# Kernel tuning notes

Hardware: AMD Instinct MI355X
Metric: run time of the kernel (lower is better)

## Reference

```python
import jax, jax.numpy as jnp
import numpy as np

DIM = 512
NUM_HEADS = 8
HEAD_DIM = DIM // NUM_HEADS
EPS = 1e-05
BETA_INIT, TEMP_INIT, SHARP_INIT = 1.0, 0.5, 4.0


def setup_inputs() -> dict:
    key = jax.random.key(0)
    ks = jax.random.split(key, 9)
    b, t = 2, 1024
    s = 1.0 / np.sqrt(DIM)
    inp = {
        "x": jax.random.normal(ks[0], (b, t, DIM), dtype=jnp.float32),
        "wq_k": jax.random.normal(ks[1], (DIM, DIM), dtype=jnp.float32) * s,
        "wq_b": jnp.zeros((DIM,), dtype=jnp.float32),
        "wk_k": jax.random.normal(ks[2], (DIM, DIM), dtype=jnp.float32) * s,
        "wk_b": jnp.zeros((DIM,), dtype=jnp.float32),
        "wv_k": jax.random.normal(ks[3], (DIM, DIM), dtype=jnp.float32) * s,
        "wv_b": jnp.zeros((DIM,), dtype=jnp.float32),
        "wo_k": jax.random.normal(ks[4], (DIM, DIM), dtype=jnp.float32) * s,
        "wo_b": jnp.zeros((DIM,), dtype=jnp.float32),
        "log_beta": jnp.full((NUM_HEADS,), np.log(BETA_INIT), dtype=jnp.float32),
        "log_temp": jnp.full((NUM_HEADS,), np.log(TEMP_INIT), dtype=jnp.float32),
        "log_sharp": jnp.full((NUM_HEADS,), np.log(SHARP_INIT), dtype=jnp.float32),
    }
    return inp


def _softplus(x, beta):
    return (1.0 / beta) * jnp.log(1.0 + jnp.exp(beta * x))


def _combine(a, b):
    # log-domain combine: elements m (b,h,t,n), log_N (b,h,t,p,n), log_D (b,h,t,n)
    m_x, ln_x, ld_x = a
    m_y, ln_y, ld_y = b
    m_new = jnp.maximum(m_x, m_y)
    dx = m_x - m_new
    dy = m_y - m_new
    # note: (..., None) broadcast onto (b,h,t,p,n) works because p == n == HEAD_DIM
    ln_new = jnp.logaddexp(ln_x + dx[..., None], ln_y + dy[..., None])
    ld_new = jnp.logaddexp(ld_x + dx, ld_y + dy)
    return (m_new, ln_new, ld_new)


def reference(x, wq_k, wq_b, wk_k, wk_b, wv_k, wv_b, wo_k, wo_b,
              log_beta, log_temp, log_sharp):
    b, t, _ = x.shape
    q = (x @ wq_k + wq_b).reshape(b, t, NUM_HEADS, HEAD_DIM).transpose(0, 2, 1, 3)
    k = (x @ wk_k + wk_b).reshape(b, t, NUM_HEADS, HEAD_DIM).transpose(0, 2, 1, 3)
    v = (x @ wv_k + wv_b).reshape(b, t, NUM_HEADS, HEAD_DIM).transpose(0, 2, 1, 3)

    beta = jnp.exp(log_beta)[:, None, None]   # (h,1,1)
    temp = jnp.exp(log_temp)[:, None, None]
    sharp = jnp.exp(log_sharp)[:, None, None]

    q = q / temp
    k = k / temp
    Qf = _softplus(q, beta)  # (b,h,t,n)
    Kf = _softplus(k, beta)

    m0 = jnp.log(Kf + EPS)                         # (b,h,t,n)
    N0 = jnp.einsum('bhtp,bhtn->bhtpn', v, Kf)     # (b,h,t,p,n)
    D0 = Kf                                        # (b,h,t,n)

    m_c, N_c, D_c = jax.lax.associative_scan(_combine, (m0, N0, D0), axis=2)

    Y_num = jnp.einsum('bhtp,bhtpq->bhtq', Qf, N_c)
    Y_den = jnp.einsum('bhtp,bhtp->bht', Qf, D_c)
    Y = Y_num / (Y_den[..., None] + EPS)           # (b,h,t,n)
    Y = jnp.sign(Y) * jnp.abs(Y) ** sharp

    pos = (jnp.arange(1, t + 1, dtype=Y.dtype) / t).reshape(1, 1, t, 1)
    Y = Y * pos

    Y = Y.transpose(0, 2, 1, 3).reshape(b, t, DIM)
    return Y @ wo_k + wo_b
```

## Files before the change

### kernel.cpp

```cpp
#include <hip/hip_runtime.h>
#include <hip/hip_bf16.h>
#include <math.h>

#define DIM 512
#define NH 8
#define HD 64
#define TT 1024
#define CH 64
#define CL 16
#define EPSF 1e-5f
#define LN2F 0.69314718056f
#define LOG2EF 1.44269504089f

typedef unsigned short ushort_t;
typedef __attribute__((ext_vector_type(8))) short bf16x8;
typedef __attribute__((ext_vector_type(4))) float f32x4;

__device__ __forceinline__ float fexp2(float x) { return __builtin_amdgcn_exp2f(x); }
__device__ __forceinline__ float flog2(float x) { return __builtin_amdgcn_logf(x); }

__device__ __forceinline__ ushort_t f2bf(float f) {
    union { float f; unsigned u; } v; v.f = f;
    unsigned r = v.u + 0x7FFFu + ((v.u >> 16) & 1u);
    return (ushort_t)(r >> 16);
}
__device__ __forceinline__ float bf2f(ushort_t h) {
    union { unsigned u; float f; } v; v.u = ((unsigned)h) << 16;
    return v.f;
}

__launch_bounds__(256)
__global__ void k_cvt_x(const float* __restrict__ x, ushort_t* __restrict__ xh,
                        ushort_t* __restrict__ xl)
{
    int i = (blockIdx.x * 256 + threadIdx.x) * 4;
    float4 v = *(const float4*)&x[i];
    ushort4 h, l;
    h.x = f2bf(v.x); l.x = f2bf(v.x - bf2f(h.x));
    h.y = f2bf(v.y); l.y = f2bf(v.y - bf2f(h.y));
    h.z = f2bf(v.z); l.z = f2bf(v.z - bf2f(h.z));
    h.w = f2bf(v.w); l.w = f2bf(v.w - bf2f(h.w));
    *(ushort4*)&xh[i] = h;
    *(ushort4*)&xl[i] = l;
}

__launch_bounds__(256)
__global__ void k_cvt_w(const float* __restrict__ wq, const float* __restrict__ wk,
                        const float* __restrict__ wv, const float* __restrict__ wo,
                        ushort_t* __restrict__ wTh, ushort_t* __restrict__ wTl,
                        ushort_t* __restrict__ wTo)
{
    const int mat = blockIdx.z;
    const float* w = (mat == 0) ? wq : (mat == 1) ? wk : (mat == 2) ? wv : wo;
    const int n  = blockIdx.x * 64 + (threadIdx.x & 63);
    const int k0 = blockIdx.y * 128 + (threadIdx.x >> 6) * 32;

    ushort_t hb[32], lb[32];
#pragma unroll
    for (int j = 0; j < 32; j++) {
        float v = w[(size_t)(k0 + j) * DIM + n];
        hb[j] = f2bf(v);
        lb[j] = f2bf(v - bf2f(hb[j]));
    }
    if (mat < 3) {
        ushort_t* dh = wTh + (size_t)mat * DIM * DIM + (size_t)n * DIM + k0;
        ushort_t* dl = wTl + (size_t)mat * DIM * DIM + (size_t)n * DIM + k0;
#pragma unroll
        for (int j = 0; j < 8; j++) {
            ushort4 th = { hb[4*j], hb[4*j+1], hb[4*j+2], hb[4*j+3] };
            ushort4 tl = { lb[4*j], lb[4*j+1], lb[4*j+2], lb[4*j+3] };
            *(ushort4*)&dh[4*j] = th;
            *(ushort4*)&dl[4*j] = tl;
        }
    } else {
        ushort_t* dh = wTo + (size_t)n * DIM + k0;
#pragma unroll
        for (int j = 0; j < 8; j++) {
            ushort4 th = { hb[4*j], hb[4*j+1], hb[4*j+2], hb[4*j+3] };
            *(ushort4*)&dh[4*j] = th;
        }
    }
}

__launch_bounds__(256, 4)
__global__ void k_gemm_qkv(const ushort_t* __restrict__ xh, const ushort_t* __restrict__ xl,
                           const ushort_t* __restrict__ wTh, const ushort_t* __restrict__ wTl,
                           const float* __restrict__ bq, const float* __restrict__ bk,
                           const float* __restrict__ bv,
                           const float* __restrict__ lbeta, const float* __restrict__ ltemp,
                           float* __restrict__ Qf2, float* __restrict__ Kf,
                           float* __restrict__ Vv2)
{
    const int z = blockIdx.z, h = blockIdx.x;
    const int rowBase = blockIdx.y * 64;
    const int colBase = h * 64;
    const float* bias = (z == 0) ? bq : (z == 1) ? bk : bv;

    __shared__ __align__(16) ushort_t lds[2][4][2048];

    const int tid = threadIdx.x;
    const int l = tid & 63, wv = tid >> 6;
    const int m = l & 15, g = l >> 4;

    const int rl = tid >> 2, cc = tid & 3;
    const int ci = ((rl >> 4) * 64 + cc * 16 + (rl & 15)) * 8;
    const ushort_t* gAh = xh + (size_t)(rowBase + rl) * DIM + cc * 8;
    const ushort_t* gAl = xl + (size_t)(rowBase + rl) * DIM + cc * 8;
    const ushort_t* gBh = wTh + (size_t)z * DIM * DIM + (size_t)(colBase + rl) * DIM + cc * 8;
    const ushort_t* gBl = wTl + (size_t)z * DIM * DIM + (size_t)(colBase + rl) * DIM + cc * 8;

    f32x4 acc[4] = { {0,0,0,0}, {0,0,0,0}, {0,0,0,0}, {0,0,0,0} };

    {
        bf16x8 a0 = *(const bf16x8*)gAh;
        bf16x8 a1 = *(const bf16x8*)gAl;
        bf16x8 b0 = *(const bf16x8*)gBh;
        bf16x8 b1 = *(const bf16x8*)gBl;
        *(bf16x8*)&lds[0][0][ci] = a0;
        *(bf16x8*)&lds[0][1][ci] = a1;
        *(bf16x8*)&lds[0][2][ci] = b0;
        *(bf16x8*)&lds[0][3][ci] = b1;
    }
    __syncthreads();

    for (int it = 0; it < 16; ++it) {
        const int cur = it & 1;
        bf16x8 nAh, nAl, nBh, nBl;
        if (it < 15) {
            const int K = (it + 1) * 32;
            nAh = *(const bf16x8*)(gAh + K);
            nAl = *(const bf16x8*)(gAl + K);
            nBh = *(const bf16x8*)(gBh + K);
            nBl = *(const bf16x8*)(gBl + K);
        }
        bf16x8 ah = *(const bf16x8*)&lds[cur][0][tid * 8];
        bf16x8 al = *(const bf16x8*)&lds[cur][1][tid * 8];
#pragma unroll
        for (int n = 0; n < 4; n++) {
            bf16x8 bh = *(const bf16x8*)&lds[cur][2][(n * 64 + l) * 8];
            bf16x8 bl = *(const bf16x8*)&lds[cur][3][(n * 64 + l) * 8];
            acc[n] = __builtin_amdgcn_mfma_f32_16x16x32_bf16(ah, bh, acc[n], 0, 0, 0);
            acc[n] = __builtin_amdgcn_mfma_f32_16x16x32_bf16(al, bh, acc[n], 0, 0, 0);
            acc[n] = __builtin_amdgcn_mfma_f32_16x16x32_bf16(ah, bl, acc[n], 0, 0, 0);
        }
        if (it < 15) {
            const int nxt = cur ^ 1;
            *(bf16x8*)&lds[nxt][0][ci] = nAh;
            *(bf16x8*)&lds[nxt][1][ci] = nAl;
            *(bf16x8*)&lds[nxt][2][ci] = nBh;
            *(bf16x8*)&lds[nxt][3][ci] = nBl;
            __syncthreads();
        }
    }

    if (z == 2) {
#pragma unroll
        for (int n = 0; n < 4; n++) {
            int c = n * 16 + m;
            float bval = bias[colBase + c];
#pragma unroll
            for (int r = 0; r < 4; r++) {
                int rr = rowBase + wv * 16 + g * 4 + r;
                int bb = rr >> 10, t = rr & (TT - 1);
                Vv2[(((size_t)(bb * NH + h)) * TT + t) * HD + c] = (acc[n][r] + bval) * LOG2EF;
            }
        }
    } else {
        float beta = expf(lbeta[h]);
        float itemp = 1.0f / expf(ltemp[h]);
        float oscale = (z == 0) ? (LN2F / beta) : (1.0f / beta);
        float* __restrict__ dst = (z == 0) ? Qf2 : Kf;
#pragma unroll
        for (int n = 0; n < 4; n++) {
            int c = n * 16 + m;
            float bval = bias[colBase + c];
#pragma unroll
            for (int r = 0; r < 4; r++) {
                int rr = rowBase + wv * 16 + g * 4 + r;
                int bb = rr >> 10, t = rr & (TT - 1);
                float val = (acc[n][r] + bval) * itemp;
                float zz = beta * val;
                float sp = (fmaxf(zz, 0.f) + log1pf(expf(-fabsf(zz)))) * oscale;
                dst[(((size_t)(bb * NH + h)) * TT + t) * HD + c] = sp;
            }
        }
    }
}

__launch_bounds__(256)
__global__ void k_chunk_reduce(const float* __restrict__ Kf, const float* __restrict__ Vv2,
                               float* __restrict__ aA, float* __restrict__ aD,
                               float* __restrict__ aCM)
{
    const int c = blockIdx.x >> 1, qh = blockIdx.x & 1;
    const int bh = blockIdx.z * NH + blockIdx.y;
    const int tid = threadIdx.x;

    __shared__ __align__(16) float sK[CL * HD];
    __shared__ __align__(16) float sV2[CL * HD];
    __shared__ __align__(16) float sM02[CL * HD];

    size_t base = ((size_t)bh * TT + (size_t)c * CL) * HD;
    const float4* K4 = (const float4*)(Kf + base);
    const float4* V4 = (const float4*)(Vv2 + base);
    {
        int f = tid;
        float4 kv = K4[f];
        ((float4*)sK)[f] = kv;
        float4 mm;
        mm.x = flog2(kv.x + EPSF); mm.y = flog2(kv.y + EPSF);
        mm.z = flog2(kv.z + EPSF); mm.w = flog2(kv.w + EPSF);
        ((float4*)sM02)[f] = mm;
        ((float4*)sV2)[f] = V4[f];
    }
    __syncthreads();

    const int p = tid & 63, qo = tid >> 6;
    const int q0 = qh * 32 + qo * 8;
    float A[8] = {};
    float AD = 0.f, cmx = 0.f;
    const bool doD = (qh == 0) && (tid < 64);

    for (int s = 0; s < CL; s++) {
        float vp = sV2[s * HD + p];
        float mp = sM02[s * HD + p];
        float4 ka = *(const float4*)&sK[s * HD + q0];
        float4 kb = *(const float4*)&sK[s * HD + q0 + 4];
        A[0] += fexp2(fmaf(vp, ka.x, mp));
        A[1] += fexp2(fmaf(vp, ka.y, mp));
        A[2] += fexp2(fmaf(vp, ka.z, mp));
        A[3] += fexp2(fmaf(vp, ka.w, mp));
        A[4] += fexp2(fmaf(vp, kb.x, mp));
        A[5] += fexp2(fmaf(vp, kb.y, mp));
        A[6] += fexp2(fmaf(vp, kb.z, mp));
        A[7] += fexp2(fmaf(vp, kb.w, mp));
        if (doD) {
            float kn = sK[s * HD + tid];
            float mn = sM02[s * HD + tid];
            AD += fexp2(fmaf(kn, LOG2EF, mn));
            cmx = fmaxf(cmx, kn + EPSF);
        }
    }

    size_t abase = ((size_t)bh * CH + c) * 4096 + (size_t)p * HD + q0;
    float4 o0 = { A[0], A[1], A[2], A[3] };
    float4 o1 = { A[4], A[5], A[6], A[7] };
    *(float4*)&aA[abase] = o0;
    *(float4*)&aA[abase + 4] = o1;
    if (doD) {
        size_t dbase = ((size_t)bh * CH + c) * HD + tid;
        aD[dbase] = AD; aCM[dbase] = cmx;
    }
}

__global__ void k_scan_agg(float* __restrict__ aA, float* __restrict__ aD,
                           float* __restrict__ aCM, int BH)
{
    int idx = blockIdx.x * 256 + threadIdx.x;
    int nA4 = BH * 1024;
    int nD4 = BH * 16;
    if (idx < nA4) {
        int bh = idx >> 10, pn4 = (idx & 1023) * 4;
        float4 Sr = {0.f, 0.f, 0.f, 0.f};
        for (int c = 0; c < CH; c++) {
            float* p = &aA[((size_t)bh * CH + c) * 4096 + pn4];
            float4 t = *(float4*)p;
            *(float4*)p = Sr;
            Sr.x += t.x; Sr.y += t.y; Sr.z += t.z; Sr.w += t.w;
        }
    } else if (idx < nA4 + nD4) {
        int i = idx - nA4; int bh = i >> 4, n4 = (i & 15) * 4;
        float4 Sr = {0.f, 0.f, 0.f, 0.f};
        for (int c = 0; c < CH; c++) {
            float* p = &aD[((size_t)bh * CH + c) * HD + n4];
            float4 t = *(float4*)p;
            *(float4*)p = Sr;
            Sr.x += t.x; Sr.y += t.y; Sr.z += t.z; Sr.w += t.w;
        }
    } else if (idx < nA4 + 2 * nD4) {
        int i = idx - nA4 - nD4; int bh = i >> 4, n4 = (i & 15) * 4;
        float4 r = {0.f, 0.f, 0.f, 0.f};
        for (int c = 0; c < CH; c++) {
            float* p = &aCM[((size_t)bh * CH + c) * HD + n4];
            float4 t = *(float4*)p;
            *(float4*)p = r;
            r.x = fmaxf(r.x, t.x); r.y = fmaxf(r.y, t.y);
            r.z = fmaxf(r.z, t.z); r.w = fmaxf(r.w, t.w);
        }
    }
}

__launch_bounds__(64)
__global__ void k_den(const float* __restrict__ Kf, const float* __restrict__ Qf2,
                      const float* __restrict__ aD, const float* __restrict__ aCM,
                      float* __restrict__ c1f, float* __restrict__ invd)
{
    const int c = blockIdx.x;
    const int bh = blockIdx.z * NH + blockIdx.y;
    const int n = threadIdx.x;
    size_t dbase = ((size_t)bh * CH + c) * HD + n;
    float AD = aD[dbase], cmx = aCM[dbase];
    size_t base = ((size_t)bh * TT + (size_t)c * CL) * HD + n;
    float* outc = c1f + (size_t)bh * TT + c * CL;
    float* outi = invd + (size_t)bh * TT + c * CL;

    for (int s = 0; s < CL; s++) {
        float kn = Kf[base + (size_t)s * HD];
        float qn = Qf2[base + (size_t)s * HD];
        float mn = flog2(kn + EPSF);
        AD += fexp2(fmaf(kn, LOG2EF, mn));
        cmx = fmaxf(cmx, kn + EPSF);
        float t1 = qn * flog2(cmx);
        float t2 = qn * flog2(AD);
#pragma unroll
        for (int off = 1; off <= 32; off <<= 1) {
            t1 += __shfl_xor(t1, off);
            t2 += __shfl_xor(t2, off);
        }
        if (n == 0) {
            outc[s] = t1;
            outi[s] = 1.0f / (t2 - t1 + EPSF);
        }
    }
}

__launch_bounds__(256)
__global__ void k_chunk_out(const float* __restrict__ Kf, const float* __restrict__ Vv2,
                            const float* __restrict__ Qf2, const float* __restrict__ aA,
                            const float* __restrict__ c1f, const float* __restrict__ invd,
                            const float* __restrict__ lsharp, ushort_t* __restrict__ Ymb)
{
    const int c = blockIdx.x, hh = blockIdx.y, bb = blockIdx.z;
    const int bh = bb * NH + hh;
    const int tid = threadIdx.x;

    __shared__ __align__(16) float sK[CL * HD];
    __shared__ __align__(16) float sV2[CL * HD];
    __shared__ __align__(16) float sM02[CL * HD];
    __shared__ __align__(16) float sQ2[CL * HD];

    size_t base = ((size_t)bh * TT + (size_t)c * CL) * HD;
    const float4* K4 = (const float4*)(Kf + base);
    const float4* V4 = (const float4*)(Vv2 + base);
    const float4* Q4 = (const float4*)(Qf2 + base);
    {
        int f = tid;
        float4 kv = K4[f];
        ((float4*)sK)[f] = kv;
        float4 mm;
        mm.x = flog2(kv.x + EPSF); mm.y = flog2(kv.y + EPSF);
        mm.z = flog2(kv.z + EPSF); mm.w = flog2(kv.w + EPSF);
        ((float4*)sM02)[f] = mm;
        ((float4*)sV2)[f] = V4[f];
        ((float4*)sQ2)[f] = Q4[f];
    }
    __syncthreads();

    const int lane = tid & 63, w = tid >> 6;
    const int g = lane >> 3, qil = lane & 7;
    const int qA = w * 8 + qil, qB = qA + 32;
    const int p0 = g * 8;

    float A[8], Bq[8];
    size_t abase = ((size_t)bh * CH + c) * 4096;
#pragma unroll
    for (int j = 0; j < 8; j++) {
        A[j]  = aA[abase + (size_t)(p0 + j) * HD + qA];
        Bq[j] = aA[abase + (size_t)(p0 + j) * HD + qB];
    }
    const float sharp = expf(lsharp[hh]);
    const float invT = 1.0f / (float)TT;
    const float* c1p = c1f + (size_t)bh * TT + c * CL;
    const float* ivp = invd + (size_t)bh * TT + c * CL;

    for (int s = 0; s < CL; s++) {
        float kqA = sK[s * HD + qA];
        float kqB = sK[s * HD + qB];
        float pA0 = 0.f, pA1 = 0.f, pB0 = 0.f, pB1 = 0.f;
#pragma unroll
        for (int j4 = 0; j4 < 2; j4++) {
            float4 vv = *(const float4*)&sV2[s * HD + p0 + j4 * 4];
            float4 mm = *(const float4*)&sM02[s * HD + p0 + j4 * 4];
            float4 qv = *(const float4*)&sQ2[s * HD + p0 + j4 * 4];
#define STEP(comp, jj, PA, PB) { \
            A[jj]  += fexp2(fmaf(vv.comp, kqA, mm.comp)); \
            PA = fmaf(qv.comp, flog2(A[jj]), PA); \
            Bq[jj] += fexp2(fmaf(vv.comp, kqB, mm.comp)); \
            PB = fmaf(qv.comp, flog2(Bq[jj]), PB); }
            STEP(x, j4 * 4 + 0, pA0, pB0)
            STEP(y, j4 * 4 + 1, pA1, pB1)
            STEP(z, j4 * 4 + 2, pA0, pB0)
            STEP(w, j4 * 4 + 3, pA1, pB1)
#undef STEP
        }
        float partA = pA0 + pA1;
        float partB = pB0 + pB1;
        partA += __shfl_xor(partA, 8);
        partA += __shfl_xor(partA, 16);
        partA += __shfl_xor(partA, 32);
        partB += __shfl_xor(partB, 8);
        partB += __shfl_xor(partB, 16);
        partB += __shfl_xor(partB, 32);

        float c1v = c1p[s], iv = ivp[s];
        int tg = c * CL + s;
        float scale = (float)(tg + 1) * invT;
        float yA = (partA - c1v) * iv;
        float yB = (partB - c1v) * iv;
        float oA = copysignf(fexp2(sharp * flog2(fabsf(yA))), yA) * scale;
        float oB = copysignf(fexp2(sharp * flog2(fabsf(yB))), yB) * scale;
        if (g == 0) {
            ushort_t* yrow = Ymb + ((size_t)(bb * TT + tg)) * DIM + hh * HD;
            yrow[qA] = f2bf(oA);
            yrow[qB] = f2bf(oB);
        }
    }
}

__launch_bounds__(256, 4)
__global__ void k_gemm_out(const ushort_t* __restrict__ Ymb, const ushort_t* __restrict__ wTo,
                           const float* __restrict__ bias, float* __restrict__ out)
{
    const int colBase = blockIdx.x * 64;
    const int rowBase = blockIdx.y * 32;

    __shared__ __align__(16) ushort_t sA[2][1024];
    __shared__ __align__(16) ushort_t sB[2][2048];

    const int tid = threadIdx.x;
    const int l = tid & 63, wv = tid >> 6;
    const int m = l & 15, g = l >> 4;
    const int wr = wv & 1, wc = wv >> 1;

    const int rlB = tid >> 2, ccB = tid & 3;
    const int ciB = ((rlB >> 4) * 64 + ccB * 16 + (rlB & 15)) * 8;
    const ushort_t* gB = wTo + (size_t)(colBase + rlB) * DIM + ccB * 8;
    const int rlA = (tid & 127) >> 2, ccA = tid & 3;
    const int ciA = ((rlA >> 4) * 64 + ccA * 16 + (rlA & 15)) * 8;
    const ushort_t* gA = Ymb + (size_t)(rowBase + rlA) * DIM + ccA * 8;
    const bool doA = tid < 128;

    f32x4 acc[2] = { {0,0,0,0}, {0,0,0,0} };

    {
        bf16x8 b0 = *(const bf16x8*)gB;
        *(bf16x8*)&sB[0][ciB] = b0;
        if (doA) {
            bf16x8 a0 = *(const bf16x8*)gA;
            *(bf16x8*)&sA[0][ciA] = a0;
        }
    }
    __syncthreads();

    for (int it = 0; it < 16; ++it) {
        const int cur = it & 1;
        bf16x8 nA, nB;
        if (it < 15) {
            const int K = (it + 1) * 32;
            nB = *(const bf16x8*)(gB + K);
            if (doA) nA = *(const bf16x8*)(gA + K);
        }
        bf16x8 a = *(const bf16x8*)&sA[cur][(wr * 64 + l) * 8];
#pragma unroll
        for (int n = 0; n < 2; n++) {
            bf16x8 b = *(const bf16x8*)&sB[cur][((wc * 2 + n) * 64 + l) * 8];
            acc[n] = __builtin_amdgcn_mfma_f32_16x16x32_bf16(a, b, acc[n], 0, 0, 0);
        }
        if (it < 15) {
            const int nxt = cur ^ 1;
            *(bf16x8*)&sB[nxt][ciB] = nB;
            if (doA) *(bf16x8*)&sA[nxt][ciA] = nA;
            __syncthreads();
        }
    }

#pragma unroll
    for (int n = 0; n < 2; n++) {
        int c = colBase + wc * 32 + n * 16 + m;
        float bval = bias[c];
#pragma unroll
        for (int r = 0; r < 4; r++) {
            int rr = rowBase + wr * 16 + g * 4 + r;
            out[(size_t)rr * DIM + c] = acc[n][r] + bval;
        }
    }
}

extern "C" void kernel_launch(void* const* d_in, const int* in_sizes, int n_in,
                              void* d_out, int out_size, void* d_ws, size_t ws_size,
                              hipStream_t stream)
{
    const float* x  = (const float*)d_in[0];
    const float* wq = (const float*)d_in[1];
    const float* bq = (const float*)d_in[2];
    const float* wk = (const float*)d_in[3];
    const float* bk = (const float*)d_in[4];
    const float* wv = (const float*)d_in[5];
    const float* bv = (const float*)d_in[6];
    const float* wo = (const float*)d_in[7];
    const float* bo = (const float*)d_in[8];
    const float* lb = (const float*)d_in[9];
    const float* lt = (const float*)d_in[10];
    const float* ls = (const float*)d_in[11];

    const int B  = in_sizes[0] / (TT * DIM);
    const int BH = B * NH;

    float* ws = (float*)d_ws;
    const size_t nQ = (size_t)BH * TT * HD;
    float* Qf2 = ws;
    float* Kf  = Qf2 + nQ;
    float* Vv2 = Kf + nQ;
    float* region = Vv2 + nQ;

    ushort_t* xh  = (ushort_t*)region;
    ushort_t* xl  = xh + (size_t)B * TT * DIM;
    ushort_t* wTh = (ushort_t*)(region + (size_t)B * TT * DIM);
    ushort_t* wTl = wTh + (size_t)3 * DIM * DIM;
    ushort_t* Ymb = (ushort_t*)region;
    float* aA  = region + (size_t)B * TT * DIM;
    float* aD  = aA  + (size_t)BH * CH * 4096;
    float* aCM = aD  + (size_t)BH * CH * HD;
    float* c1f = aCM + (size_t)BH * CH * HD;
    float* invd= c1f + (size_t)BH * TT;
    ushort_t* wTo = (ushort_t*)(invd + (size_t)BH * TT);

    k_cvt_x<<<(B * TT * DIM) / 1024, 256, 0, stream>>>(x, xh, xl);

    dim3 gw(DIM / 64, DIM / 128, 4);
    k_cvt_w<<<gw, 256, 0, stream>>>(wq, wk, wv, wo, wTh, wTl, wTo);

    dim3 g1(NH, (B * TT) / 64, 3);
    k_gemm_qkv<<<g1, 256, 0, stream>>>(xh, xl, wTh, wTl, bq, bk, bv, lb, lt, Qf2, Kf, Vv2);

    dim3 g2(CH * 2, NH, B);
    k_chunk_reduce<<<g2, 256, 0, stream>>>(Kf, Vv2, aA, aD, aCM);

    int ntot = BH * 1024 + 2 * BH * 16;
    k_scan_agg<<<(ntot + 255) / 256, 256, 0, stream>>>(aA, aD, aCM, BH);

    dim3 g4(CH, NH, B);
    k_den<<<g4, 64, 0, stream>>>(Kf, Qf2, aD, aCM, c1f, invd);

    k_chunk_out<<<g4, 256, 0, stream>>>(Kf, Vv2, Qf2, aA, c1f, invd, ls, Ymb);

    dim3 g6(DIM / 64, (B * TT) / 32);
    k_gemm_out<<<g6, 256, 0, stream>>>(Ymb, wTo, bo, (float*)d_out);
}
```

Baseline: 98.63 us.

## Parallelize chunk-prefix scan across wave lanes and per-token denominator

The serial per-thread scan over 64 chunks is replaced by a wave-level shuffle scan, with one wave per (bh, pn4) column and the chunk index mapped to the lane. The denominator kernel is restructured from one 64-thread block per chunk with a serial loop over 16 tokens to one thread per (token, 8-feature group), where each thread recomputes the within-chunk prefix. exp(k)*log2(k+eps) is also simplified to exp2(k*log2e)*(k+eps), which drops a log. The cost is many more waves and redundant recomputation inside each chunk, and the chunk-strided loads in the scan are uncoalesced.

```diff
diff --git a/kernel.cpp b/kernel.cpp
--- a/kernel.cpp
+++ b/kernel.cpp
@@ -236,9 +236,9 @@
         A[7] += fexp2(fmaf(vp, kb.w, mp));
         if (doD) {
             float kn = sK[s * HD + tid];
-            float mn = sM02[s * HD + tid];
-            AD += fexp2(fmaf(kn, LOG2EF, mn));
-            cmx = fmaxf(cmx, kn + EPSF);
+            float ke = kn + EPSF;
+            AD += fexp2(kn * LOG2EF) * ke;
+            cmx = fmaxf(cmx, ke);
         }
     }
 
@@ -253,74 +253,120 @@
     }
 }
 
-__global__ void k_scan_agg(float* __restrict__ aA, float* __restrict__ aD,
-                           float* __restrict__ aCM, int BH)
-{
-    int idx = blockIdx.x * 256 + threadIdx.x;
-    int nA4 = BH * 1024;
-    int nD4 = BH * 16;
-    if (idx < nA4) {
-        int bh = idx >> 10, pn4 = (idx & 1023) * 4;
-        float4 Sr = {0.f, 0.f, 0.f, 0.f};
-        for (int c = 0; c < CH; c++) {
-            float* p = &aA[((size_t)bh * CH + c) * 4096 + pn4];
-            float4 t = *(float4*)p;
-            *(float4*)p = Sr;
-            Sr.x += t.x; Sr.y += t.y; Sr.z += t.z; Sr.w += t.w;
-        }
-    } else if (idx < nA4 + nD4) {
-        int i = idx - nA4; int bh = i >> 4, n4 = (i & 15) * 4;
-        float4 Sr = {0.f, 0.f, 0.f, 0.f};
-        for (int c = 0; c < CH; c++) {
-            float* p = &aD[((size_t)bh * CH + c) * HD + n4];
-            float4 t = *(float4*)p;
-            *(float4*)p = Sr;
-            Sr.x += t.x; Sr.y += t.y; Sr.z += t.z; Sr.w += t.w;
-        }
-    } else if (idx < nA4 + 2 * nD4) {
-        int i = idx - nA4 - nD4; int bh = i >> 4, n4 = (i & 15) * 4;
-        float4 r = {0.f, 0.f, 0.f, 0.f};
-        for (int c = 0; c < CH; c++) {
-            float* p = &aCM[((size_t)bh * CH + c) * HD + n4];
-            float4 t = *(float4*)p;
-            *(float4*)p = r;
-            r.x = fmaxf(r.x, t.x); r.y = fmaxf(r.y, t.y);
-            r.z = fmaxf(r.z, t.z); r.w = fmaxf(r.w, t.w);
-        }
-    }
-}
-
-__launch_bounds__(64)
+__launch_bounds__(256)
+__global__ void k_scan_wave(float* __restrict__ aA, float* __restrict__ aD,
+                            float* __restrict__ aCM, int BH)
+{
+    const int wid = (blockIdx.x * 256 + threadIdx.x) >> 6;
+    const int lane = threadIdx.x & 63;
+    const int nA = BH * 1024, nD = BH * 16;
+
+    if (wid < nA) {
+        int bh = wid >> 10, pn4 = wid & 1023;
+        float* p = &aA[((size_t)(bh * CH + lane)) * 4096 + pn4 * 4];
+        float4 v = *(float4*)p;
+#pragma unroll
+        for (int off = 1; off < 64; off <<= 1) {
+            float ux = __shfl_up(v.x, off);
+            float uy = __shfl_up(v.y, off);
+            float uz = __shfl_up(v.z, off);
+            float uw = __shfl_up(v.w, off);
+            if (lane >= off) { v.x += ux; v.y += uy; v.z += uz; v.w += uw; }
+        }
+        float4 e;
+        e.x = __shfl_up(v.x, 1); e.y = __shfl_up(v.y, 1);
+        e.z = __shfl_up(v.z, 1); e.w = __shfl_up(v.w, 1);
+        if (lane == 0) { e.x = 0.f; e.y = 0.f; e.z = 0.f; e.w = 0.f; }
+        *(float4*)p = e;
+    } else if (wid < nA + nD) {
+        int i = wid - nA; int bh = i >> 4, n4 = i & 15;
+        float* p = &aD[((size_t)(bh * CH + lane)) * HD + n4 * 4];
+        float4 v = *(float4*)p;
+#pragma unroll
+        for (int off = 1; off < 64; off <<= 1) {
+            float ux = __shfl_up(v.x, off);
+            float uy = __shfl_up(v.y, off);
+            float uz = __shfl_up(v.z, off);
+            float uw = __shfl_up(v.w, off);
+            if (lane >= off) { v.x += ux; v.y += uy; v.z += uz; v.w += uw; }
+        }
+        float4 e;
+        e.x = __shfl_up(v.x, 1); e.y = __shfl_up(v.y, 1);
+        e.z = __shfl_up(v.z, 1); e.w = __shfl_up(v.w, 1);
+        if (lane == 0) { e.x = 0.f; e.y = 0.f; e.z = 0.f; e.w = 0.f; }
+        *(float4*)p = e;
+    } else if (wid < nA + 2 * nD) {
+        int i = wid - nA - nD; int bh = i >> 4, n4 = i & 15;
+        float* p = &aCM[((size_t)(bh * CH + lane)) * HD + n4 * 4];
+        float4 v = *(float4*)p;
+#pragma unroll
+        for (int off = 1; off < 64; off <<= 1) {
+            float ux = __shfl_up(v.x, off);
+            float uy = __shfl_up(v.y, off);
+            float uz = __shfl_up(v.z, off);
+            float uw = __shfl_up(v.w, off);
+            if (lane >= off) {
+                v.x = fmaxf(v.x, ux); v.y = fmaxf(v.y, uy);
+                v.z = fmaxf(v.z, uz); v.w = fmaxf(v.w, uw);
+            }
+        }
+        float4 e;
+        e.x = __shfl_up(v.x, 1); e.y = __shfl_up(v.y, 1);
+        e.z = __shfl_up(v.z, 1); e.w = __shfl_up(v.w, 1);
+        if (lane == 0) { e.x = 0.f; e.y = 0.f; e.z = 0.f; e.w = 0.f; }
+        *(float4*)p = e;
+    }
+}
+
+__launch_bounds__(256)
 __global__ void k_den(const float* __restrict__ Kf, const float* __restrict__ Qf2,
                       const float* __restrict__ aD, const float* __restrict__ aCM,
                       float* __restrict__ c1f, float* __restrict__ invd)
 {
-    const int c = blockIdx.x;
-    const int bh = blockIdx.z * NH + blockIdx.y;
-    const int n = threadIdx.x;
-    size_t dbase = ((size_t)bh * CH + c) * HD + n;
-    float AD = aD[dbase], cmx = aCM[dbase];
-    size_t base = ((size_t)bh * TT + (size_t)c * CL) * HD + n;
-    float* outc = c1f + (size_t)bh * TT + c * CL;
-    float* outi = invd + (size_t)bh * TT + c * CL;
-
-    for (int s = 0; s < CL; s++) {
-        float kn = Kf[base + (size_t)s * HD];
-        float qn = Qf2[base + (size_t)s * HD];
-        float mn = flog2(kn + EPSF);
-        AD += fexp2(fmaf(kn, LOG2EF, mn));
-        cmx = fmaxf(cmx, kn + EPSF);
-        float t1 = qn * flog2(cmx);
-        float t2 = qn * flog2(AD);
-#pragma unroll
-        for (int off = 1; off <= 32; off <<= 1) {
-            t1 += __shfl_xor(t1, off);
-            t2 += __shfl_xor(t2, off);
-        }
-        if (n == 0) {
-            outc[s] = t1;
-            outi[s] = 1.0f / (t2 - t1 + EPSF);
-        }
+    const int idx = blockIdx.x * 256 + threadIdx.x;
+    const int bh = idx >> 13;
+    const int t  = (idx >> 3) & 1023;
+    const int ng = idx & 7;
+    const int c = t >> 4, tc = t & 15;
+    const int n0 = ng * 8;
+
+    size_t dofs = ((size_t)(bh * CH + c)) * HD + n0;
+    float AD[8], cm[8];
+    *(float4*)&AD[0] = *(const float4*)&aD[dofs];
+    *(float4*)&AD[4] = *(const float4*)&aD[dofs + 4];
+    *(float4*)&cm[0] = *(const float4*)&aCM[dofs];
+    *(float4*)&cm[4] = *(const float4*)&aCM[dofs + 4];
+
+    size_t kbase = ((size_t)(bh * TT + c * CL)) * HD + n0;
+    for (int s = 0; s <= tc; s++) {
+        float k4[8];
+        *(float4*)&k4[0] = *(const float4*)&Kf[kbase + (size_t)s * HD];
+        *(float4*)&k4[4] = *(const float4*)&Kf[kbase + (size_t)s * HD + 4];
+#pragma unroll
+        for (int j = 0; j < 8; j++) {
+            float ke = k4[j] + EPSF;
+            AD[j] += fexp2(k4[j] * LOG2EF) * ke;
+            cm[j] = fmaxf(cm[j], ke);
+        }
+    }
+
+    float q4[8];
+    size_t qofs = ((size_t)(bh * TT + t)) * HD + n0;
+    *(float4*)&q4[0] = *(const float4*)&Qf2[qofs];
+    *(float4*)&q4[4] = *(const float4*)&Qf2[qofs + 4];
+
+    float t1 = 0.f, t2 = 0.f;
+#pragma unroll
+    for (int j = 0; j < 8; j++) {
+        t1 = fmaf(q4[j], flog2(cm[j]), t1);
+        t2 = fmaf(q4[j], flog2(AD[j]), t2);
+    }
+    t1 += __shfl_xor(t1, 1); t1 += __shfl_xor(t1, 2); t1 += __shfl_xor(t1, 4);
+    t2 += __shfl_xor(t2, 1); t2 += __shfl_xor(t2, 2); t2 += __shfl_xor(t2, 4);
+
+    if (ng == 0) {
+        c1f[(size_t)bh * TT + t] = t1;
+        invd[(size_t)bh * TT + t] = 1.0f / (t2 - t1 + EPSF);
     }
 }
 
@@ -536,12 +582,12 @@
     dim3 g2(CH * 2, NH, B);
     k_chunk_reduce<<<g2, 256, 0, stream>>>(Kf, Vv2, aA, aD, aCM);
 
-    int ntot = BH * 1024 + 2 * BH * 16;
-    k_scan_agg<<<(ntot + 255) / 256, 256, 0, stream>>>(aA, aD, aCM, BH);
+    int nwaves = BH * 1024 + 2 * BH * 16;
+    k_scan_wave<<<(nwaves + 3) / 4, 256, 0, stream>>>(aA, aD, aCM, BH);
+
+    k_den<<<(BH * TT * 8) / 256, 256, 0, stream>>>(Kf, Qf2, aD, aCM, c1f, invd);
 
     dim3 g4(CH, NH, B);
-    k_den<<<g4, 64, 0, stream>>>(Kf, Qf2, aD, aCM, c1f, invd);
-
     k_chunk_out<<<g4, 256, 0, stream>>>(Kf, Vv2, Qf2, aA, c1f, invd, ls, Ymb);
 
     dim3 g6(DIM / 64, (B * TT) / 32);
```

Result: slower. 105.0 us (+6.4%).
